# Kernel tuning notes

Hardware: AMD Instinct MI355X
Metric: run time of the kernel (lower is better)

Reference implementation:

```python
import jax, jax.numpy as jnp
import numpy as np

NUM_ATOMS = 100
D = 32        # initial_atom_dim
H = 16        # hidden_dim (multiplicity per irrep)
NB = 16       # edge_dim / number of bessel basis functions
CUT = 6.0     # radius_cutoff
DEG = 4.0     # degree_norm
OUT = 1       # output_dim
INV4PI = 1.0 / np.sqrt(4.0 * np.pi)  # 'integral' SH normalization


def _bessel(d, nb, cut):
    # e3nn soft_one_hot_linspace(basis='bessel', cutoff=True) * sqrt(nb)
    x = d[:, None]
    n = jnp.arange(1, nb + 1, dtype=d.dtype)
    safe = jnp.maximum(x, 1e-9)
    out = np.sqrt(2.0 / cut) * jnp.sin(n * jnp.pi * x / cut) / safe
    return out * (x < cut) * np.sqrt(float(nb))


def _fc(x, w1, w2):
    # e3nn FullyConnectedNet: fan-in normalized linear layers, silu, no bias
    h = jax.nn.silu(x @ w1 / np.sqrt(x.shape[-1]))
    return h @ w2 / np.sqrt(w1.shape[-1])


def _forward(atomic_numbers, edge_index, coords, atom_emb,
             fc0_w1, fc0_w2, fc1_w1, fc1_w2, w_readout):
    src, dst = edge_index[0], edge_index[1]
    N = coords.shape[0]
    E = src.shape[0]

    vec = coords[src] - coords[dst]                      # [E,3]
    dist = jnp.linalg.norm(vec, axis=-1)                 # [E]
    unit = vec / jnp.maximum(dist, 1e-9)[:, None]

    # spherical harmonics, l=0 and l=1, 'integral' normalization
    y0 = jnp.full((E,), INV4PI, dtype=coords.dtype)      # [E]
    y1 = (np.sqrt(3.0) * INV4PI) * unit                  # [E,3]
    basis = _bessel(dist, NB, CUT)                       # [E,NB]

    x = atom_emb[atomic_numbers]                         # [N,D] (row 0 is padding)

    # ---- layer 0: scalars (D x0e) x (1x0e+1x1o) -> H x0e + H x1o ----
    w = _fc(basis, fc0_w1, fc0_w2)                       # [E, 2*D*H] per-edge TP weights
    wa = w[:, : D * H].reshape(E, D, H)
    wb = w[:, D * H:].reshape(E, D, H)
    xs = x[src]
    n0 = 1.0 / np.sqrt(D)                                # path fan-in norm
    m0 = jnp.einsum('ed,edh->eh', xs, wa) * y0[:, None] * n0          # [E,H]
    m1 = jnp.einsum('ed,edh->eh', xs, wb)[:, :, None] * y1[:, None, :] * n0  # [E,H,3]
    z0 = jax.ops.segment_sum(m0, dst, num_segments=N) / DEG           # [N,H]
    z1 = jax.ops.segment_sum(m1, dst, num_segments=N) / DEG           # [N,H,3]

    # ---- layer 1: (H x0e + H x1o) x (1x0e+1x1o) -> same irreps, skip-connected ----
    w = _fc(basis, fc1_w1, fc1_w2)                       # [E, 4*H*H]
    w1_ = w[:, 0 * H * H:1 * H * H].reshape(E, H, H)     # 0e x 0e -> 0e
    w2_ = w[:, 1 * H * H:2 * H * H].reshape(E, H, H)     # 0e x 1o -> 1o
    w3_ = w[:, 2 * H * H:3 * H * H].reshape(E, H, H)     # 1o x 0e -> 1o
    w4_ = w[:, 3 * H * H:4 * H * H].reshape(E, H, H)     # 1o x 1o -> 0e (CG = dot/sqrt(3))
    s, v = z0[src], z1[src]
    n1 = 1.0 / np.sqrt(2 * H)                            # two paths per output irrep
    dot = jnp.einsum('ehm,em->eh', v, y1) / np.sqrt(3.0)
    o0 = (jnp.einsum('eh,ehk->ek', s, w1_) * y0[:, None]
          + jnp.einsum('eh,ehk->ek', dot, w4_)) * n1
    o1 = (jnp.einsum('eh,ehk->ek', s, w2_)[:, :, None] * y1[:, None, :]
          + jnp.einsum('ehm,ehk->ekm', v, w3_) * y0[:, None, None]) * n1
    z0 = jax.ops.segment_sum(o0, dst, num_segments=N) / DEG + z0      # skip
    z1 = jax.ops.segment_sum(o1, dst, num_segments=N) / DEG + z1

    # ---- scalar readout (o3.Linear onto 0e) + graph sum-pool ----
    node_scalar = z0 @ w_readout / np.sqrt(H)            # [N,OUT]
    return jnp.sum(node_scalar, axis=0)                  # [OUT]


def setup_inputs() -> dict:
    key = jax.random.key(0)
    ks = jax.random.split(key, 9)
    N, E = 10000, 160000
    atomic_numbers = jax.random.randint(ks[0], (N,), 0, NUM_ATOMS)
    coords = jax.random.normal(ks[1], (N, 3), dtype=jnp.float32)
    edge_index = jax.random.randint(ks[2], (2, E), 0, N)
    atom_emb = jax.random.normal(ks[3], (NUM_ATOMS, D), dtype=jnp.float32).at[0].set(0.0)
    fc0_w1 = jax.random.normal(ks[4], (NB, H), dtype=jnp.float32)
    fc0_w2 = jax.random.normal(ks[5], (H, 2 * D * H), dtype=jnp.float32)
    fc1_w1 = jax.random.normal(ks[6], (NB, H), dtype=jnp.float32)
    fc1_w2 = jax.random.normal(ks[7], (H, 4 * H * H), dtype=jnp.float32)
    w_readout = jax.random.normal(ks[8], (H, OUT), dtype=jnp.float32)
    return {"atomic_numbers": atomic_numbers, "coords": coords, "edge_index": edge_index,
            "atom_emb": atom_emb, "fc0_w1": fc0_w1, "fc0_w2": fc0_w2,
            "fc1_w1": fc1_w1, "fc1_w2": fc1_w2, "w_readout": w_readout}


def reference(atomic_numbers, coords, edge_index, atom_emb,
              fc0_w1, fc0_w2, fc1_w1, fc1_w2, w_readout):
    return _forward(atomic_numbers, edge_index, coords, atom_emb,
                    fc0_w1, fc0_w2, fc1_w1, fc1_w2, w_readout)
```

## Files before the change

### kernel.cpp

```cpp
#include <hip/hip_runtime.h>
#include <math.h>


namespace {
constexpr int   NATOMS   = 100;
constexpr float PI_F     = 3.14159265358979323846f;
constexpr float INV4PI_F = 0.28209479177387814f;
constexpr float SQRT3_F  = 1.7320508075688772f;
constexpr float CUT_F    = 6.0f;
constexpr float BASIS_C  = 2.3094010767585034f;
constexpr float N0_F     = 0.17677669529663687f;
constexpr float K0_F = INV4PI_F * N0_F * 0.0625f;
constexpr float K1_F = SQRT3_F * INV4PI_F * N0_F * 0.0625f;
constexpr float P2SC = INV4PI_F * N0_F * (1.0f / 64.0f);
}

__device__ __forceinline__ float silu_fast(float x) {
  return x / (1.0f + __expf(-x));
}

__device__ __forceinline__ float block_reduce_sum(float v) {
  #pragma unroll
  for (int o = 32; o > 0; o >>= 1) v += __shfl_down(v, o, 64);
  __shared__ float ls[8];
  int lane = threadIdx.x & 63;
  int w    = threadIdx.x >> 6;
  if (lane == 0) ls[w] = v;
  __syncthreads();
  float s = 0.f;
  if (threadIdx.x == 0) {
    int nw = (blockDim.x + 63) >> 6;
    for (int i = 0; i < nw; ++i) s += ls[i];
  }
  return s;
}

__global__ void table_kernel(const float* __restrict__ atom_emb,
                             const float* __restrict__ fc0_w2,
                             const float* __restrict__ fc1_w2,
                             const float* __restrict__ w_readout,
                             float* __restrict__ TI,
                             float* __restrict__ G1T, float* __restrict__ G4T,
                             float* __restrict__ zacc,
                             float* __restrict__ out,
                             int N64) {
  int b = blockIdx.x;
  int tt = threadIdx.x;
  if (b < NATOMS) {
    int j = tt >> 4;
    int h = tt & 15;
    float s0 = 0.f, s1 = 0.f;
    #pragma unroll
    for (int d = 0; d < 32; ++d) {
      float x = atom_emb[b * 32 + d];
      s0 = fmaf(x, fc0_w2[j * 1024 + d * 16 + h], s0);
      s1 = fmaf(x, fc0_w2[j * 1024 + 512 + d * 16 + h], s1);
    }
    TI[b * 512 + j * 32 + 2 * h]     = s0;
    TI[b * 512 + j * 32 + 2 * h + 1] = s1;
  } else if (b == NATOMS) {
    int j = tt >> 4;
    int h = tt & 15;
    float g1 = 0.f, g4 = 0.f;
    #pragma unroll
    for (int k = 0; k < 16; ++k) {
      float r = w_readout[k];
      g1 = fmaf(fc1_w2[j * 1024 + h * 16 + k], r, g1);
      g4 = fmaf(fc1_w2[j * 1024 + 768 + h * 16 + k], r, g4);
    }
    G1T[h * 16 + j] = g1;
    G4T[h * 16 + j] = g4;
    if (tt == 0) *out = 0.f;
  } else {
    int idx = (b - NATOMS - 1) * 256 + tt;
    if (idx < N64) zacc[idx] = 0.f;
  }
}

__global__ void __launch_bounds__(256)
edge_kernel(const int* __restrict__ ei,
            const float* __restrict__ coords,
            const int* __restrict__ an,
            const float* __restrict__ TI,
            const float* __restrict__ fc0_w1,
            const float* __restrict__ fc1_w1,
            float* __restrict__ zacc,
            float* __restrict__ hbuf,
            float4* __restrict__ ubuf,
            int E) {
  int lane = threadIdx.x & 63;
  int g    = threadIdx.x >> 4;
  int t    = threadIdx.x & 15;
  int base = lane & 48;

  float w0c[16], w1c[16];
  #pragma unroll
  for (int k = 0; k < 16; ++k) {
    w0c[k] = fc0_w1[k * 16 + t];
    w1c[k] = fc1_w1[k * 16 + t];
  }

  const float angc = PI_F / CUT_F;
  int eA = blockIdx.x * 32 + g;
  int eB = eA + 16;
  bool vA = eA < E, vB = eB < E;
  int eAc = vA ? eA : 0, eBc = vB ? eB : 0;

  int sA = ei[eAc], dA = ei[E + eAc];
  int sB = ei[eBc], dB = ei[E + eBc];
  float sxA = coords[3 * sA + 0], syA = coords[3 * sA + 1], szA = coords[3 * sA + 2];
  float dxA = coords[3 * dA + 0], dyA = coords[3 * dA + 1], dzA = coords[3 * dA + 2];
  float sxB = coords[3 * sB + 0], syB = coords[3 * sB + 1], szB = coords[3 * sB + 2];
  float dxB = coords[3 * dB + 0], dyB = coords[3 * dB + 1], dzB = coords[3 * dB + 2];
  int aA = an[sA], aB = an[sB];

  float vxA = sxA - dxA, vyA = syA - dyA, vzA = szA - dzA;
  float vxB = sxB - dxB, vyB = syB - dyB, vzB = szB - dzB;
  float distA = sqrtf(vxA * vxA + vyA * vyA + vzA * vzA);
  float distB = sqrtf(vxB * vxB + vyB * vyB + vzB * vzB);
  float ivA = 1.0f / fmaxf(distA, 1e-9f);
  float ivB = 1.0f / fmaxf(distB, 1e-9f);
  float uxA = vxA * ivA, uyA = vyA * ivA, uzA = vzA * ivA;
  float uxB = vxB * ivB, uyB = vyB * ivB, uzB = vzB * ivB;
  float bcA = (distA < CUT_F) ? (BASIS_C * ivA) : 0.0f;
  float bcB = (distB < CUT_F) ? (BASIS_C * ivB) : 0.0f;

  if (t == 0) {
    if (vA) ubuf[eA] = make_float4(uxA, uyA, uzA, 0.f);
    if (vB) ubuf[eB] = make_float4(uxB, uyB, uzB, 0.f);
  }

  float angA = angc * distA, angB = angc * distB;
  float scA = __sinf(angA), twA = 2.0f * __cosf(angA), spA = 0.f;
  float scB = __sinf(angB), twB = 2.0f * __cosf(angB), spB = 0.f;
  float a0A = 0.f, a1A = 0.f, a0B = 0.f, a1B = 0.f;
  #pragma unroll
  for (int k = 0; k < 16; ++k) {
    a0A = fmaf(scA, w0c[k], a0A);
    a1A = fmaf(scA, w1c[k], a1A);
    a0B = fmaf(scB, w0c[k], a0B);
    a1B = fmaf(scB, w1c[k], a1B);
    float snA = fmaf(twA, scA, -spA); spA = scA; scA = snA;
    float snB = fmaf(twB, scB, -spB); spB = scB; scB = snB;
  }
  float h0A = silu_fast(a0A * bcA * 0.25f);
  float h1A = silu_fast(a1A * bcA * 0.25f);
  float h0B = silu_fast(a0B * bcB * 0.25f);
  float h1B = silu_fast(a1B * bcB * 0.25f);

  if (vA) hbuf[(size_t)eA * 16 + t] = h1A;
  if (vB) hbuf[(size_t)eB * 16 + t] = h1B;

  const float2* tpA = (const float2*)(TI + aA * 512) + t;
  const float2* tpB = (const float2*)(TI + aB * 512) + t;
  float u0A = 0.f, u1A = 0.f, u0B = 0.f, u1B = 0.f;
  #pragma unroll
  for (int j = 0; j < 16; ++j) {
    float hjA = __shfl(h0A, base + j, 64);
    float hjB = __shfl(h0B, base + j, 64);
    float2 TA = tpA[j * 16];
    float2 TB = tpB[j * 16];
    u0A = fmaf(hjA, TA.x, u0A);
    u1A = fmaf(hjA, TA.y, u1A);
    u0B = fmaf(hjB, TB.x, u0B);
    u1B = fmaf(hjB, TB.y, u1B);
  }

  if (vA) {
    float* za = zacc + (size_t)dA * 64 + t;
    float m1 = K1_F * u1A;
    unsafeAtomicAdd(za,      K0_F * u0A);
    unsafeAtomicAdd(za + 16, m1 * uxA);
    unsafeAtomicAdd(za + 32, m1 * uyA);
    unsafeAtomicAdd(za + 48, m1 * uzA);
  }
  if (vB) {
    float* zb = zacc + (size_t)dB * 64 + t;
    float m1 = K1_F * u1B;
    unsafeAtomicAdd(zb,      K0_F * u0B);
    unsafeAtomicAdd(zb + 16, m1 * uxB);
    unsafeAtomicAdd(zb + 32, m1 * uyB);
    unsafeAtomicAdd(zb + 48, m1 * uzB);
  }
}

__global__ void __launch_bounds__(256)
node_qp_kernel(const float* __restrict__ zacc,
               const float* __restrict__ G1T,
               const float* __restrict__ G4T,
               const float* __restrict__ w_readout,
               float* __restrict__ QP,
               float* __restrict__ out,
               int N) {
  __shared__ float ggs[512];
  ggs[threadIdx.x]       = G1T[threadIdx.x];
  ggs[256 + threadIdx.x] = G4T[threadIdx.x];
  __syncthreads();

  int lane = threadIdx.x & 63;
  int t    = lane & 15;
  int base = lane & 48;
  int node = blockIdx.x * 16 + (threadIdx.x >> 4);
  bool valid = node < N;
  size_t nb = (size_t)(valid ? node : 0) * 64;

  float z0 = zacc[nb + t];
  float zx = zacc[nb + 16 + t];
  float zy = zacc[nb + 32 + t];
  float zz = zacc[nb + 48 + t];

  float Q = 0.f, Px = 0.f, Py = 0.f, Pz = 0.f;
  #pragma unroll
  for (int h = 0; h < 16; ++h) {
    float z0h = __shfl(z0, base + h, 64);
    float zxh = __shfl(zx, base + h, 64);
    float zyh = __shfl(zy, base + h, 64);
    float zzh = __shfl(zz, base + h, 64);
    float g1 = ggs[h * 16 + t];
    float g4 = ggs[256 + h * 16 + t];
    Q  = fmaf(g1, z0h, Q);
    Px = fmaf(g4, zxh, Px);
    Py = fmaf(g4, zyh, Py);
    Pz = fmaf(g4, zzh, Pz);
  }
  if (valid) {
    QP[nb + t]      = Q;
    QP[nb + 16 + t] = Px;
    QP[nb + 32 + t] = Py;
    QP[nb + 48 + t] = Pz;
  }

  float c = valid ? 0.25f * z0 * w_readout[t] : 0.f;
  float tot = block_reduce_sum(c);
  if (threadIdx.x == 0) atomicAdd(out, tot);
}

__global__ void __launch_bounds__(256)
edge2_kernel(const int* __restrict__ ei,
             const float4* __restrict__ ubuf,
             const float* __restrict__ hbuf,
             const float* __restrict__ QP,
             float* __restrict__ out,
             int E) {
  int t  = threadIdx.x & 15;
  int gg = blockIdx.x * 16 + (threadIdx.x >> 4);
  int ngroups = gridDim.x * 16;

  float c = 0.f;
  for (int e = gg; e < E; e += ngroups) {
    int s = ei[e];
    float4 u = ubuf[e];
    float h1 = hbuf[(size_t)e * 16 + t];
    size_t sb = (size_t)s * 64;
    float Qt  = QP[sb + t];
    float Pxt = QP[sb + 16 + t];
    float Pyt = QP[sb + 32 + t];
    float Pzt = QP[sb + 48 + t];
    c = fmaf(h1, fmaf(Pxt, u.x, fmaf(Pyt, u.y, fmaf(Pzt, u.z, Qt))), c);
  }
  c *= P2SC;
  float tot = block_reduce_sum(c);
  if (threadIdx.x == 0) atomicAdd(out, tot);
}

extern "C" void kernel_launch(void* const* d_in, const int* in_sizes, int n_in,
                              void* d_out, int out_size, void* d_ws, size_t ws_size,
                              hipStream_t stream) {
  const int*   an        = (const int*)d_in[0];
  const float* coords    = (const float*)d_in[1];
  const int*   ei        = (const int*)d_in[2];
  const float* atom_emb  = (const float*)d_in[3];
  const float* fc0_w1    = (const float*)d_in[4];
  const float* fc0_w2    = (const float*)d_in[5];
  const float* fc1_w1    = (const float*)d_in[6];
  const float* fc1_w2    = (const float*)d_in[7];
  const float* w_readout = (const float*)d_in[8];

  int N = in_sizes[0];
  int E = in_sizes[2] / 2;
  int N64 = N * 64;

  float4* ubuf = (float4*)d_ws;
  float*  hbuf = (float*)(ubuf + E);
  float*  zacc = hbuf + (size_t)E * 16;
  float*  QP   = zacc + N64;
  float*  TI   = QP + N64;
  float*  G1T  = TI + NATOMS * 512;
  float*  G4T  = G1T + 256;
  float*  out  = (float*)d_out;

  int blk = 256;
  int zgrid = (N64 + blk - 1) / blk;
  table_kernel<<<NATOMS + 1 + zgrid, blk, 0, stream>>>(
      atom_emb, fc0_w2, fc1_w2, w_readout, TI, G1T, G4T, zacc, out, N64);

  edge_kernel<<<(E + 31) / 32, blk, 0, stream>>>(
      ei, coords, an, TI, fc0_w1, fc1_w1, zacc, hbuf, ubuf, E);

  node_qp_kernel<<<(N + 15) / 16, blk, 0, stream>>>(
      zacc, G1T, G4T, w_readout, QP, out, N);

  edge2_kernel<<<2048, blk, 0, stream>>>(ei, ubuf, hbuf, QP, out, E);
}
```

Baseline: 161.0 us.

## Fuse all stages into one cooperative persistent kernel with grid syncs

```diff
diff --git a/kernel.cpp b/kernel.cpp
--- a/kernel.cpp
+++ b/kernel.cpp
@@ -1,6 +1,9 @@
 #include <hip/hip_runtime.h>
+#include <hip/hip_cooperative_groups.h>
 #include <math.h>
 
+
+namespace cg = cooperative_groups;
 
 namespace {
 constexpr int   NATOMS   = 100;
@@ -35,232 +38,250 @@
   return s;
 }
 
-__global__ void table_kernel(const float* __restrict__ atom_emb,
-                             const float* __restrict__ fc0_w2,
-                             const float* __restrict__ fc1_w2,
-                             const float* __restrict__ w_readout,
-                             float* __restrict__ TI,
-                             float* __restrict__ G1T, float* __restrict__ G4T,
-                             float* __restrict__ zacc,
-                             float* __restrict__ out,
-                             int N64) {
-  int b = blockIdx.x;
-  int tt = threadIdx.x;
-  if (b < NATOMS) {
-    int j = tt >> 4;
-    int h = tt & 15;
-    float s0 = 0.f, s1 = 0.f;
+__global__ void __launch_bounds__(256)
+fused_kernel(const int* __restrict__ an,
+             const float* __restrict__ coords,
+             const int* __restrict__ ei,
+             const float* __restrict__ atom_emb,
+             const float* __restrict__ fc0_w1,
+             const float* __restrict__ fc0_w2,
+             const float* __restrict__ fc1_w1,
+             const float* __restrict__ fc1_w2,
+             const float* __restrict__ w_readout,
+             float* __restrict__ TI,
+             float* __restrict__ G1T,
+             float* __restrict__ G4T,
+             float* __restrict__ zacc,
+             float* __restrict__ QP,
+             float* __restrict__ out,
+             int N, int E) {
+  cg::grid_group grid = cg::this_grid();
+  const int tt     = threadIdx.x;
+  const int lane   = tt & 63;
+  const int t      = tt & 15;
+  const int base   = lane & 48;
+  const int ggid   = blockIdx.x * 16 + (tt >> 4);
+  const int ngroups = gridDim.x * 16;
+  const float angc = PI_F / CUT_F;
+
+  {
+    float4* z4 = (float4*)zacc;
+    int n4 = N * 16;
+    for (int i = blockIdx.x * 256 + tt; i < n4; i += gridDim.x * 256)
+      z4[i] = make_float4(0.f, 0.f, 0.f, 0.f);
+    if (blockIdx.x == 0 && tt == 0) *out = 0.f;
+
+    for (int task = ggid; task < NATOMS * 16 + 16; task += ngroups) {
+      if (task < NATOMS * 16) {
+        int b = task >> 4, j = task & 15;
+        float s0 = 0.f, s1 = 0.f;
+        #pragma unroll
+        for (int d = 0; d < 32; ++d) {
+          float x = atom_emb[b * 32 + d];
+          s0 = fmaf(x, fc0_w2[j * 1024 + d * 16 + t], s0);
+          s1 = fmaf(x, fc0_w2[j * 1024 + 512 + d * 16 + t], s1);
+        }
+        TI[b * 512 + j * 32 + 2 * t]     = s0;
+        TI[b * 512 + j * 32 + 2 * t + 1] = s1;
+      } else {
+        int j = task - NATOMS * 16;
+        float g1 = 0.f, g4 = 0.f;
+        #pragma unroll
+        for (int k = 0; k < 16; ++k) {
+          float r = w_readout[k];
+          g1 = fmaf(fc1_w2[j * 1024 + t * 16 + k], r, g1);
+          g4 = fmaf(fc1_w2[j * 1024 + 768 + t * 16 + k], r, g4);
+        }
+        G1T[t * 16 + j] = g1;
+        G4T[t * 16 + j] = g4;
+      }
+    }
+  }
+  grid.sync();
+
+  {
+    float w0c[16];
     #pragma unroll
-    for (int d = 0; d < 32; ++d) {
-      float x = atom_emb[b * 32 + d];
-      s0 = fmaf(x, fc0_w2[j * 1024 + d * 16 + h], s0);
-      s1 = fmaf(x, fc0_w2[j * 1024 + 512 + d * 16 + h], s1);
+    for (int k = 0; k < 16; ++k) w0c[k] = fc0_w1[k * 16 + t];
+
+    for (int e0 = ggid; e0 < E; e0 += 2 * ngroups) {
+      int eA = e0;
+      int eB = e0 + ngroups;
+      bool vB = eB < E;
+      int eBc = vB ? eB : eA;
+
+      int sA = ei[eA],  dA = ei[E + eA];
+      int sB = ei[eBc], dB = ei[E + eBc];
+      float sxA = coords[3 * sA + 0], syA = coords[3 * sA + 1], szA = coords[3 * sA + 2];
+      float dxA = coords[3 * dA + 0], dyA = coords[3 * dA + 1], dzA = coords[3 * dA + 2];
+      float sxB = coords[3 * sB + 0], syB = coords[3 * sB + 1], szB = coords[3 * sB + 2];
+      float dxB = coords[3 * dB + 0], dyB = coords[3 * dB + 1], dzB = coords[3 * dB + 2];
+      int aA = an[sA], aB = an[sB];
+
+      float vxA = sxA - dxA, vyA = syA - dyA, vzA = szA - dzA;
+      float vxB = sxB - dxB, vyB = syB - dyB, vzB = szB - dzB;
+      float distA = sqrtf(vxA * vxA + vyA * vyA + vzA * vzA);
+      float distB = sqrtf(vxB * vxB + vyB * vyB + vzB * vzB);
+      float ivA = 1.0f / fmaxf(distA, 1e-9f);
+      float ivB = 1.0f / fmaxf(distB, 1e-9f);
+      float uxA = vxA * ivA, uyA = vyA * ivA, uzA = vzA * ivA;
+      float uxB = vxB * ivB, uyB = vyB * ivB, uzB = vzB * ivB;
+      float bcA = (distA < CUT_F) ? (BASIS_C * ivA) : 0.0f;
+      float bcB = (distB < CUT_F) ? (BASIS_C * ivB) : 0.0f;
+
+      float angA = angc * distA, angB = angc * distB;
+      float scA = __sinf(angA), twA = 2.0f * __cosf(angA), spA = 0.f;
+      float scB = __sinf(angB), twB = 2.0f * __cosf(angB), spB = 0.f;
+      float a0A = 0.f, a0B = 0.f;
+      #pragma unroll
+      for (int k = 0; k < 16; ++k) {
+        a0A = fmaf(scA, w0c[k], a0A);
+        a0B = fmaf(scB, w0c[k], a0B);
+        float snA = fmaf(twA, scA, -spA); spA = scA; scA = snA;
+        float snB = fmaf(twB, scB, -spB); spB = scB; scB = snB;
+      }
+      float h0A = silu_fast(a0A * bcA * 0.25f);
+      float h0B = silu_fast(a0B * bcB * 0.25f);
+
+      const float2* tpA = (const float2*)(TI + aA * 512) + t;
+      const float2* tpB = (const float2*)(TI + aB * 512) + t;
+      float u0A = 0.f, u1A = 0.f, u0B = 0.f, u1B = 0.f;
+      #pragma unroll
+      for (int j = 0; j < 16; ++j) {
+        float hjA = __shfl(h0A, base + j, 64);
+        float hjB = __shfl(h0B, base + j, 64);
+        float2 TA = tpA[j * 16];
+        float2 TB = tpB[j * 16];
+        u0A = fmaf(hjA, TA.x, u0A);
+        u1A = fmaf(hjA, TA.y, u1A);
+        u0B = fmaf(hjB, TB.x, u0B);
+        u1B = fmaf(hjB, TB.y, u1B);
+      }
+
+      {
+        float* za = zacc + (size_t)dA * 64 + t;
+        float m1 = K1_F * u1A;
+        unsafeAtomicAdd(za,      K0_F * u0A);
+        unsafeAtomicAdd(za + 16, m1 * uxA);
+        unsafeAtomicAdd(za + 32, m1 * uyA);
+        unsafeAtomicAdd(za + 48, m1 * uzA);
+      }
+      if (vB) {
+        float* zb = zacc + (size_t)dB * 64 + t;
+        float m1 = K1_F * u1B;
+        unsafeAtomicAdd(zb,      K0_F * u0B);
+        unsafeAtomicAdd(zb + 16, m1 * uxB);
+        unsafeAtomicAdd(zb + 32, m1 * uyB);
+        unsafeAtomicAdd(zb + 48, m1 * uzB);
+      }
     }
-    TI[b * 512 + j * 32 + 2 * h]     = s0;
-    TI[b * 512 + j * 32 + 2 * h + 1] = s1;
-  } else if (b == NATOMS) {
-    int j = tt >> 4;
-    int h = tt & 15;
-    float g1 = 0.f, g4 = 0.f;
+  }
+  grid.sync();
+
+  __shared__ float ggs[512];
+  ggs[tt]       = G1T[tt];
+  ggs[256 + tt] = G4T[tt];
+  __syncthreads();
+
+  float rsum = 0.f;
+  {
+    float rr = w_readout[t];
+    for (int n = ggid; n < N; n += ngroups) {
+      size_t nb = (size_t)n * 64;
+      float z0 = zacc[nb + t];
+      float zx = zacc[nb + 16 + t];
+      float zy = zacc[nb + 32 + t];
+      float zz = zacc[nb + 48 + t];
+
+      float Q = 0.f, Px = 0.f, Py = 0.f, Pz = 0.f;
+      #pragma unroll
+      for (int h = 0; h < 16; ++h) {
+        float z0h = __shfl(z0, base + h, 64);
+        float zxh = __shfl(zx, base + h, 64);
+        float zyh = __shfl(zy, base + h, 64);
+        float zzh = __shfl(zz, base + h, 64);
+        float g1 = ggs[h * 16 + t];
+        float g4 = ggs[256 + h * 16 + t];
+        Q  = fmaf(g1, z0h, Q);
+        Px = fmaf(g4, zxh, Px);
+        Py = fmaf(g4, zyh, Py);
+        Pz = fmaf(g4, zzh, Pz);
+      }
+      QP[nb + t]      = Q;
+      QP[nb + 16 + t] = Px;
+      QP[nb + 32 + t] = Py;
+      QP[nb + 48 + t] = Pz;
+      rsum = fmaf(0.25f * z0, rr, rsum);
+    }
+  }
+  grid.sync();
+
+  float c3 = 0.f;
+  {
+    float w1c[16];
     #pragma unroll
-    for (int k = 0; k < 16; ++k) {
-      float r = w_readout[k];
-      g1 = fmaf(fc1_w2[j * 1024 + h * 16 + k], r, g1);
-      g4 = fmaf(fc1_w2[j * 1024 + 768 + h * 16 + k], r, g4);
+    for (int k = 0; k < 16; ++k) w1c[k] = fc1_w1[k * 16 + t];
+
+    for (int e0 = ggid; e0 < E; e0 += 2 * ngroups) {
+      int eA = e0;
+      int eB = e0 + ngroups;
+      bool vB = eB < E;
+      int eBc = vB ? eB : eA;
+
+      int sA = ei[eA],  dA = ei[E + eA];
+      int sB = ei[eBc], dB = ei[E + eBc];
+      float sxA = coords[3 * sA + 0], syA = coords[3 * sA + 1], szA = coords[3 * sA + 2];
+      float dxA = coords[3 * dA + 0], dyA = coords[3 * dA + 1], dzA = coords[3 * dA + 2];
+      float sxB = coords[3 * sB + 0], syB = coords[3 * sB + 1], szB = coords[3 * sB + 2];
+      float dxB = coords[3 * dB + 0], dyB = coords[3 * dB + 1], dzB = coords[3 * dB + 2];
+
+      float vxA = sxA - dxA, vyA = syA - dyA, vzA = szA - dzA;
+      float vxB = sxB - dxB, vyB = syB - dyB, vzB = szB - dzB;
+      float distA = sqrtf(vxA * vxA + vyA * vyA + vzA * vzA);
+      float distB = sqrtf(vxB * vxB + vyB * vyB + vzB * vzB);
+      float ivA = 1.0f / fmaxf(distA, 1e-9f);
+      float ivB = 1.0f / fmaxf(distB, 1e-9f);
+      float uxA = vxA * ivA, uyA = vyA * ivA, uzA = vzA * ivA;
+      float uxB = vxB * ivB, uyB = vyB * ivB, uzB = vzB * ivB;
+      float bcA = (distA < CUT_F) ? (BASIS_C * ivA) : 0.0f;
+      float bcB = (distB < CUT_F) ? (BASIS_C * ivB) : 0.0f;
+
+      float angA = angc * distA, angB = angc * distB;
+      float scA = __sinf(angA), twA = 2.0f * __cosf(angA), spA = 0.f;
+      float scB = __sinf(angB), twB = 2.0f * __cosf(angB), spB = 0.f;
+      float a1A = 0.f, a1B = 0.f;
+      #pragma unroll
+      for (int k = 0; k < 16; ++k) {
+        a1A = fmaf(scA, w1c[k], a1A);
+        a1B = fmaf(scB, w1c[k], a1B);
+        float snA = fmaf(twA, scA, -spA); spA = scA; scA = snA;
+        float snB = fmaf(twB, scB, -spB); spB = scB; scB = snB;
+      }
+      float h1A = silu_fast(a1A * bcA * 0.25f);
+      float h1B = silu_fast(a1B * bcB * 0.25f);
+
+      {
+        size_t qa = (size_t)sA * 64;
+        float Qt  = QP[qa + t];
+        float Pxt = QP[qa + 16 + t];
+        float Pyt = QP[qa + 32 + t];
+        float Pzt = QP[qa + 48 + t];
+        c3 = fmaf(h1A, fmaf(Pxt, uxA, fmaf(Pyt, uyA, fmaf(Pzt, uzA, Qt))), c3);
+      }
+      if (vB) {
+        size_t qb = (size_t)sB * 64;
+        float Qt  = QP[qb + t];
+        float Pxt = QP[qb + 16 + t];
+        float Pyt = QP[qb + 32 + t];
+        float Pzt = QP[qb + 48 + t];
+        c3 = fmaf(h1B, fmaf(Pxt, uxB, fmaf(Pyt, uyB, fmaf(Pzt, uzB, Qt))), c3);
+      }
     }
-    G1T[h * 16 + j] = g1;
-    G4T[h * 16 + j] = g4;
-    if (tt == 0) *out = 0.f;
-  } else {
-    int idx = (b - NATOMS - 1) * 256 + tt;
-    if (idx < N64) zacc[idx] = 0.f;
-  }
-}
-
-__global__ void __launch_bounds__(256)
-edge_kernel(const int* __restrict__ ei,
-            const float* __restrict__ coords,
-            const int* __restrict__ an,
-            const float* __restrict__ TI,
-            const float* __restrict__ fc0_w1,
-            const float* __restrict__ fc1_w1,
-            float* __restrict__ zacc,
-            float* __restrict__ hbuf,
-            float4* __restrict__ ubuf,
-            int E) {
-  int lane = threadIdx.x & 63;
-  int g    = threadIdx.x >> 4;
-  int t    = threadIdx.x & 15;
-  int base = lane & 48;
-
-  float w0c[16], w1c[16];
-  #pragma unroll
-  for (int k = 0; k < 16; ++k) {
-    w0c[k] = fc0_w1[k * 16 + t];
-    w1c[k] = fc1_w1[k * 16 + t];
-  }
-
-  const float angc = PI_F / CUT_F;
-  int eA = blockIdx.x * 32 + g;
-  int eB = eA + 16;
-  bool vA = eA < E, vB = eB < E;
-  int eAc = vA ? eA : 0, eBc = vB ? eB : 0;
-
-  int sA = ei[eAc], dA = ei[E + eAc];
-  int sB = ei[eBc], dB = ei[E + eBc];
-  float sxA = coords[3 * sA + 0], syA = coords[3 * sA + 1], szA = coords[3 * sA + 2];
-  float dxA = coords[3 * dA + 0], dyA = coords[3 * dA + 1], dzA = coords[3 * dA + 2];
-  float sxB = coords[3 * sB + 0], syB = coords[3 * sB + 1], szB = coords[3 * sB + 2];
-  float dxB = coords[3 * dB + 0], dyB = coords[3 * dB + 1], dzB = coords[3 * dB + 2];
-  int aA = an[sA], aB = an[sB];
-
-  float vxA = sxA - dxA, vyA = syA - dyA, vzA = szA - dzA;
-  float vxB = sxB - dxB, vyB = syB - dyB, vzB = szB - dzB;
-  float distA = sqrtf(vxA * vxA + vyA * vyA + vzA * vzA);
-  float distB = sqrtf(vxB * vxB + vyB * vyB + vzB * vzB);
-  float ivA = 1.0f / fmaxf(distA, 1e-9f);
-  float ivB = 1.0f / fmaxf(distB, 1e-9f);
-  float uxA = vxA * ivA, uyA = vyA * ivA, uzA = vzA * ivA;
-  float uxB = vxB * ivB, uyB = vyB * ivB, uzB = vzB * ivB;
-  float bcA = (distA < CUT_F) ? (BASIS_C * ivA) : 0.0f;
-  float bcB = (distB < CUT_F) ? (BASIS_C * ivB) : 0.0f;
-
-  if (t == 0) {
-    if (vA) ubuf[eA] = make_float4(uxA, uyA, uzA, 0.f);
-    if (vB) ubuf[eB] = make_float4(uxB, uyB, uzB, 0.f);
-  }
-
-  float angA = angc * distA, angB = angc * distB;
-  float scA = __sinf(angA), twA = 2.0f * __cosf(angA), spA = 0.f;
-  float scB = __sinf(angB), twB = 2.0f * __cosf(angB), spB = 0.f;
-  float a0A = 0.f, a1A = 0.f, a0B = 0.f, a1B = 0.f;
-  #pragma unroll
-  for (int k = 0; k < 16; ++k) {
-    a0A = fmaf(scA, w0c[k], a0A);
-    a1A = fmaf(scA, w1c[k], a1A);
-    a0B = fmaf(scB, w0c[k], a0B);
-    a1B = fmaf(scB, w1c[k], a1B);
-    float snA = fmaf(twA, scA, -spA); spA = scA; scA = snA;
-    float snB = fmaf(twB, scB, -spB); spB = scB; scB = snB;
-  }
-  float h0A = silu_fast(a0A * bcA * 0.25f);
-  float h1A = silu_fast(a1A * bcA * 0.25f);
-  float h0B = silu_fast(a0B * bcB * 0.25f);
-  float h1B = silu_fast(a1B * bcB * 0.25f);
-
-  if (vA) hbuf[(size_t)eA * 16 + t] = h1A;
-  if (vB) hbuf[(size_t)eB * 16 + t] = h1B;
-
-  const float2* tpA = (const float2*)(TI + aA * 512) + t;
-  const float2* tpB = (const float2*)(TI + aB * 512) + t;
-  float u0A = 0.f, u1A = 0.f, u0B = 0.f, u1B = 0.f;
-  #pragma unroll
-  for (int j = 0; j < 16; ++j) {
-    float hjA = __shfl(h0A, base + j, 64);
-    float hjB = __shfl(h0B, base + j, 64);
-    float2 TA = tpA[j * 16];
-    float2 TB = tpB[j * 16];
-    u0A = fmaf(hjA, TA.x, u0A);
-    u1A = fmaf(hjA, TA.y, u1A);
-    u0B = fmaf(hjB, TB.x, u0B);
-    u1B = fmaf(hjB, TB.y, u1B);
-  }
-
-  if (vA) {
-    float* za = zacc + (size_t)dA * 64 + t;
-    float m1 = K1_F * u1A;
-    unsafeAtomicAdd(za,      K0_F * u0A);
-    unsafeAtomicAdd(za + 16, m1 * uxA);
-    unsafeAtomicAdd(za + 32, m1 * uyA);
-    unsafeAtomicAdd(za + 48, m1 * uzA);
-  }
-  if (vB) {
-    float* zb = zacc + (size_t)dB * 64 + t;
-    float m1 = K1_F * u1B;
-    unsafeAtomicAdd(zb,      K0_F * u0B);
-    unsafeAtomicAdd(zb + 16, m1 * uxB);
-    unsafeAtomicAdd(zb + 32, m1 * uyB);
-    unsafeAtomicAdd(zb + 48, m1 * uzB);
-  }
-}
-
-__global__ void __launch_bounds__(256)
-node_qp_kernel(const float* __restrict__ zacc,
-               const float* __restrict__ G1T,
-               const float* __restrict__ G4T,
-               const float* __restrict__ w_readout,
-               float* __restrict__ QP,
-               float* __restrict__ out,
-               int N) {
-  __shared__ float ggs[512];
-  ggs[threadIdx.x]       = G1T[threadIdx.x];
-  ggs[256 + threadIdx.x] = G4T[threadIdx.x];
-  __syncthreads();
-
-  int lane = threadIdx.x & 63;
-  int t    = lane & 15;
-  int base = lane & 48;
-  int node = blockIdx.x * 16 + (threadIdx.x >> 4);
-  bool valid = node < N;
-  size_t nb = (size_t)(valid ? node : 0) * 64;
-
-  float z0 = zacc[nb + t];
-  float zx = zacc[nb + 16 + t];
-  float zy = zacc[nb + 32 + t];
-  float zz = zacc[nb + 48 + t];
-
-  float Q = 0.f, Px = 0.f, Py = 0.f, Pz = 0.f;
-  #pragma unroll
-  for (int h = 0; h < 16; ++h) {
-    float z0h = __shfl(z0, base + h, 64);
-    float zxh = __shfl(zx, base + h, 64);
-    float zyh = __shfl(zy, base + h, 64);
-    float zzh = __shfl(zz, base + h, 64);
-    float g1 = ggs[h * 16 + t];
-    float g4 = ggs[256 + h * 16 + t];
-    Q  = fmaf(g1, z0h, Q);
-    Px = fmaf(g4, zxh, Px);
-    Py = fmaf(g4, zyh, Py);
-    Pz = fmaf(g4, zzh, Pz);
-  }
-  if (valid) {
-    QP[nb + t]      = Q;
-    QP[nb + 16 + t] = Px;
-    QP[nb + 32 + t] = Py;
-    QP[nb + 48 + t] = Pz;
-  }
-
-  float c = valid ? 0.25f * z0 * w_readout[t] : 0.f;
-  float tot = block_reduce_sum(c);
-  if (threadIdx.x == 0) atomicAdd(out, tot);
-}
-
-__global__ void __launch_bounds__(256)
-edge2_kernel(const int* __restrict__ ei,
-             const float4* __restrict__ ubuf,
-             const float* __restrict__ hbuf,
-             const float* __restrict__ QP,
-             float* __restrict__ out,
-             int E) {
-  int t  = threadIdx.x & 15;
-  int gg = blockIdx.x * 16 + (threadIdx.x >> 4);
-  int ngroups = gridDim.x * 16;
-
-  float c = 0.f;
-  for (int e = gg; e < E; e += ngroups) {
-    int s = ei[e];
-    float4 u = ubuf[e];
-    float h1 = hbuf[(size_t)e * 16 + t];
-    size_t sb = (size_t)s * 64;
-    float Qt  = QP[sb + t];
-    float Pxt = QP[sb + 16 + t];
-    float Pyt = QP[sb + 32 + t];
-    float Pzt = QP[sb + 48 + t];
-    c = fmaf(h1, fmaf(Pxt, u.x, fmaf(Pyt, u.y, fmaf(Pzt, u.z, Qt))), c);
-  }
-  c *= P2SC;
-  float tot = block_reduce_sum(c);
-  if (threadIdx.x == 0) atomicAdd(out, tot);
+  }
+
+  float csum = fmaf(P2SC, c3, rsum);
+  float tot = block_reduce_sum(csum);
+  if (tt == 0) atomicAdd(out, tot);
 }
 
 extern "C" void kernel_launch(void* const* d_in, const int* in_sizes, int n_in,
@@ -278,27 +299,34 @@
 
   int N = in_sizes[0];
   int E = in_sizes[2] / 2;
-  int N64 = N * 64;
-
-  float4* ubuf = (float4*)d_ws;
-  float*  hbuf = (float*)(ubuf + E);
-  float*  zacc = hbuf + (size_t)E * 16;
-  float*  QP   = zacc + N64;
-  float*  TI   = QP + N64;
-  float*  G1T  = TI + NATOMS * 512;
-  float*  G4T  = G1T + 256;
-  float*  out  = (float*)d_out;
-
-  int blk = 256;
-  int zgrid = (N64 + blk - 1) / blk;
-  table_kernel<<<NATOMS + 1 + zgrid, blk, 0, stream>>>(
-      atom_emb, fc0_w2, fc1_w2, w_readout, TI, G1T, G4T, zacc, out, N64);
-
-  edge_kernel<<<(E + 31) / 32, blk, 0, stream>>>(
-      ei, coords, an, TI, fc0_w1, fc1_w1, zacc, hbuf, ubuf, E);
-
-  node_qp_kernel<<<(N + 15) / 16, blk, 0, stream>>>(
-      zacc, G1T, G4T, w_readout, QP, out, N);
-
-  edge2_kernel<<<2048, blk, 0, stream>>>(ei, ubuf, hbuf, QP, out, E);
-}
+
+  float* zacc = (float*)d_ws;
+  float* QP   = zacc + (size_t)N * 64;
+  float* TI   = QP + (size_t)N * 64;
+  float* G1T  = TI + NATOMS * 512;
+  float* G4T  = G1T + 256;
+  float* out  = (float*)d_out;
+
+  static int coop_grid = 0;
+  if (coop_grid == 0) {
+    int mb = 0;
+    hipOccupancyMaxActiveBlocksPerMultiprocessor(&mb, fused_kernel, 256, 0);
+    if (mb < 1) mb = 1;
+    int dev = 0;
+    hipGetDevice(&dev);
+    hipDeviceProp_t prop;
+    hipGetDeviceProperties(&prop, dev);
+    int cus = prop.multiProcessorCount > 0 ? prop.multiProcessorCount : 256;
+    coop_grid = mb * cus;
+    if (coop_grid > 2048) coop_grid = 2048;
+  }
+
+  void* args[] = {
+    (void*)&an, (void*)&coords, (void*)&ei, (void*)&atom_emb,
+    (void*)&fc0_w1, (void*)&fc0_w2, (void*)&fc1_w1, (void*)&fc1_w2,
+    (void*)&w_readout, (void*)&TI, (void*)&G1T, (void*)&G4T,
+    (void*)&zacc, (void*)&QP, (void*)&out, (void*)&N, (void*)&E
+  };
+  hipLaunchCooperativeKernel((void*)fused_kernel, dim3(coop_grid), dim3(256),
+                             args, 0, stream);
+}
```

Result: slower. 330.4 us (+105.2%).

## Fold second edge pass into per-source atomic accumulators and drop edge2 kernel

Applied to the files above, without the earlier changes.

```diff
diff --git a/kernel.cpp b/kernel.cpp
--- a/kernel.cpp
+++ b/kernel.cpp
@@ -35,15 +35,13 @@
   return s;
 }
 
-__global__ void table_kernel(const float* __restrict__ atom_emb,
-                             const float* __restrict__ fc0_w2,
-                             const float* __restrict__ fc1_w2,
-                             const float* __restrict__ w_readout,
-                             float* __restrict__ TI,
-                             float* __restrict__ G1T, float* __restrict__ G4T,
-                             float* __restrict__ zacc,
-                             float* __restrict__ out,
-                             int N64) {
+__global__ void __launch_bounds__(256)
+table_kernel(const float* __restrict__ atom_emb,
+             const float* __restrict__ fc0_w2,
+             float* __restrict__ TI,
+             float4* __restrict__ zero4,
+             float* __restrict__ out,
+             int NZ4) {
   int b = blockIdx.x;
   int tt = threadIdx.x;
   if (b < NATOMS) {
@@ -58,22 +56,10 @@
     }
     TI[b * 512 + j * 32 + 2 * h]     = s0;
     TI[b * 512 + j * 32 + 2 * h + 1] = s1;
-  } else if (b == NATOMS) {
-    int j = tt >> 4;
-    int h = tt & 15;
-    float g1 = 0.f, g4 = 0.f;
-    #pragma unroll
-    for (int k = 0; k < 16; ++k) {
-      float r = w_readout[k];
-      g1 = fmaf(fc1_w2[j * 1024 + h * 16 + k], r, g1);
-      g4 = fmaf(fc1_w2[j * 1024 + 768 + h * 16 + k], r, g4);
-    }
-    G1T[h * 16 + j] = g1;
-    G4T[h * 16 + j] = g4;
-    if (tt == 0) *out = 0.f;
+    if (b == 0 && tt == 0) *out = 0.f;
   } else {
-    int idx = (b - NATOMS - 1) * 256 + tt;
-    if (idx < N64) zacc[idx] = 0.f;
+    int idx = (b - NATOMS) * 256 + tt;
+    if (idx < NZ4) zero4[idx] = make_float4(0.f, 0.f, 0.f, 0.f);
   }
 }
 
@@ -85,8 +71,7 @@
             const float* __restrict__ fc0_w1,
             const float* __restrict__ fc1_w1,
             float* __restrict__ zacc,
-            float* __restrict__ hbuf,
-            float4* __restrict__ ubuf,
+            float* __restrict__ sacc,
             int E) {
   int lane = threadIdx.x & 63;
   int g    = threadIdx.x >> 4;
@@ -125,11 +110,6 @@
   float bcA = (distA < CUT_F) ? (BASIS_C * ivA) : 0.0f;
   float bcB = (distB < CUT_F) ? (BASIS_C * ivB) : 0.0f;
 
-  if (t == 0) {
-    if (vA) ubuf[eA] = make_float4(uxA, uyA, uzA, 0.f);
-    if (vB) ubuf[eB] = make_float4(uxB, uyB, uzB, 0.f);
-  }
-
   float angA = angc * distA, angB = angc * distB;
   float scA = __sinf(angA), twA = 2.0f * __cosf(angA), spA = 0.f;
   float scB = __sinf(angB), twB = 2.0f * __cosf(angB), spB = 0.f;
@@ -148,8 +128,20 @@
   float h0B = silu_fast(a0B * bcB * 0.25f);
   float h1B = silu_fast(a1B * bcB * 0.25f);
 
-  if (vA) hbuf[(size_t)eA * 16 + t] = h1A;
-  if (vB) hbuf[(size_t)eB * 16 + t] = h1B;
+  if (vA) {
+    float* sa = sacc + (size_t)sA * 64 + t;
+    unsafeAtomicAdd(sa,      h1A);
+    unsafeAtomicAdd(sa + 16, h1A * uxA);
+    unsafeAtomicAdd(sa + 32, h1A * uyA);
+    unsafeAtomicAdd(sa + 48, h1A * uzA);
+  }
+  if (vB) {
+    float* sb = sacc + (size_t)sB * 64 + t;
+    unsafeAtomicAdd(sb,      h1B);
+    unsafeAtomicAdd(sb + 16, h1B * uxB);
+    unsafeAtomicAdd(sb + 32, h1B * uyB);
+    unsafeAtomicAdd(sb + 48, h1B * uzB);
+  }
 
   const float2* tpA = (const float2*)(TI + aA * 512) + t;
   const float2* tpB = (const float2*)(TI + aB * 512) + t;
@@ -185,16 +177,26 @@
 }
 
 __global__ void __launch_bounds__(256)
-node_qp_kernel(const float* __restrict__ zacc,
-               const float* __restrict__ G1T,
-               const float* __restrict__ G4T,
-               const float* __restrict__ w_readout,
-               float* __restrict__ QP,
-               float* __restrict__ out,
-               int N) {
+node_kernel(const float* __restrict__ zacc,
+            const float* __restrict__ sacc,
+            const float* __restrict__ fc1_w2,
+            const float* __restrict__ w_readout,
+            float* __restrict__ out,
+            int N) {
   __shared__ float ggs[512];
-  ggs[threadIdx.x]       = G1T[threadIdx.x];
-  ggs[256 + threadIdx.x] = G4T[threadIdx.x];
+  {
+    int j = threadIdx.x >> 4;
+    int h = threadIdx.x & 15;
+    float g1 = 0.f, g4 = 0.f;
+    #pragma unroll
+    for (int k = 0; k < 16; ++k) {
+      float r = w_readout[k];
+      g1 = fmaf(fc1_w2[j * 1024 + h * 16 + k], r, g1);
+      g4 = fmaf(fc1_w2[j * 1024 + 768 + h * 16 + k], r, g4);
+    }
+    ggs[h * 16 + j]       = g1;
+    ggs[256 + h * 16 + j] = g4;
+  }
   __syncthreads();
 
   int lane = threadIdx.x & 63;
@@ -208,6 +210,10 @@
   float zx = zacc[nb + 16 + t];
   float zy = zacc[nb + 32 + t];
   float zz = zacc[nb + 48 + t];
+  float A  = sacc[nb + t];
+  float Bx = sacc[nb + 16 + t];
+  float By = sacc[nb + 32 + t];
+  float Bz = sacc[nb + 48 + t];
 
   float Q = 0.f, Px = 0.f, Py = 0.f, Pz = 0.f;
   #pragma unroll
@@ -223,42 +229,13 @@
     Py = fmaf(g4, zyh, Py);
     Pz = fmaf(g4, zzh, Pz);
   }
+
+  float c = 0.f;
   if (valid) {
-    QP[nb + t]      = Q;
-    QP[nb + 16 + t] = Px;
-    QP[nb + 32 + t] = Py;
-    QP[nb + 48 + t] = Pz;
-  }
-
-  float c = valid ? 0.25f * z0 * w_readout[t] : 0.f;
-  float tot = block_reduce_sum(c);
-  if (threadIdx.x == 0) atomicAdd(out, tot);
-}
-
-__global__ void __launch_bounds__(256)
-edge2_kernel(const int* __restrict__ ei,
-             const float4* __restrict__ ubuf,
-             const float* __restrict__ hbuf,
-             const float* __restrict__ QP,
-             float* __restrict__ out,
-             int E) {
-  int t  = threadIdx.x & 15;
-  int gg = blockIdx.x * 16 + (threadIdx.x >> 4);
-  int ngroups = gridDim.x * 16;
-
-  float c = 0.f;
-  for (int e = gg; e < E; e += ngroups) {
-    int s = ei[e];
-    float4 u = ubuf[e];
-    float h1 = hbuf[(size_t)e * 16 + t];
-    size_t sb = (size_t)s * 64;
-    float Qt  = QP[sb + t];
-    float Pxt = QP[sb + 16 + t];
-    float Pyt = QP[sb + 32 + t];
-    float Pzt = QP[sb + 48 + t];
-    c = fmaf(h1, fmaf(Pxt, u.x, fmaf(Pyt, u.y, fmaf(Pzt, u.z, Qt))), c);
-  }
-  c *= P2SC;
+    float dotp = fmaf(Q, A, fmaf(Px, Bx, fmaf(Py, By, Pz * Bz)));
+    c = fmaf(0.25f * z0, w_readout[t], P2SC * dotp);
+  }
+
   float tot = block_reduce_sum(c);
   if (threadIdx.x == 0) atomicAdd(out, tot);
 }
@@ -278,27 +255,20 @@
 
   int N = in_sizes[0];
   int E = in_sizes[2] / 2;
-  int N64 = N * 64;
-
-  float4* ubuf = (float4*)d_ws;
-  float*  hbuf = (float*)(ubuf + E);
-  float*  zacc = hbuf + (size_t)E * 16;
-  float*  QP   = zacc + N64;
-  float*  TI   = QP + N64;
-  float*  G1T  = TI + NATOMS * 512;
-  float*  G4T  = G1T + 256;
-  float*  out  = (float*)d_out;
-
-  int blk = 256;
-  int zgrid = (N64 + blk - 1) / blk;
-  table_kernel<<<NATOMS + 1 + zgrid, blk, 0, stream>>>(
-      atom_emb, fc0_w2, fc1_w2, w_readout, TI, G1T, G4T, zacc, out, N64);
-
-  edge_kernel<<<(E + 31) / 32, blk, 0, stream>>>(
-      ei, coords, an, TI, fc0_w1, fc1_w1, zacc, hbuf, ubuf, E);
-
-  node_qp_kernel<<<(N + 15) / 16, blk, 0, stream>>>(
-      zacc, G1T, G4T, w_readout, QP, out, N);
-
-  edge2_kernel<<<2048, blk, 0, stream>>>(ei, ubuf, hbuf, QP, out, E);
-}
+
+  float* zacc = (float*)d_ws;
+  float* sacc = zacc + (size_t)N * 64;
+  float* TI   = sacc + (size_t)N * 64;
+  float* out  = (float*)d_out;
+
+  int NZ4 = N * 32;
+  int zblocks = (NZ4 + 255) / 256;
+  table_kernel<<<NATOMS + zblocks, 256, 0, stream>>>(
+      atom_emb, fc0_w2, TI, (float4*)zacc, out, NZ4);
+
+  edge_kernel<<<(E + 31) / 32, 256, 0, stream>>>(
+      ei, coords, an, TI, fc0_w1, fc1_w1, zacc, sacc, E);
+
+  node_kernel<<<(N + 15) / 16, 256, 0, stream>>>(
+      zacc, sacc, fc1_w2, w_readout, out, N);
+}
```

New measurement: 151.5 us. 1.06x faster.
